# Kernel optimization log

Hardware: AMD Instinct MI355X
Metric: run time of the kernel (lower is better)

Reference implementation:

```python
import jax, jax.numpy as jnp
from jax import lax
import numpy as np

EPS = 1e-5

def _conv(x, w, b, s, p):
    # torch Conv2d: weight [O,I,kH,kW], NCHW
    y = lax.conv_general_dilated(x, w, (s, s), [(p, p), (p, p)],
                                 dimension_numbers=('NCHW', 'OIHW', 'NCHW'))
    return y + b[None, :, None, None]

def _convT(x, w, b, s, p):
    # torch ConvTranspose2d: weight [I,O,kH,kW]; equivalent to lhs-dilated conv
    wf = jnp.flip(w, (2, 3)).transpose(1, 0, 2, 3)  # -> [O,I,kH,kW]
    q = w.shape[2] - 1 - p
    y = lax.conv_general_dilated(x, wf, (1, 1), [(q, q), (q, q)],
                                 lhs_dilation=(s, s),
                                 dimension_numbers=('NCHW', 'OIHW', 'NCHW'))
    return y + b[None, :, None, None]

def _bn(x, g, b, m, v):
    # eval-mode BatchNorm2d with running stats
    s = g / jnp.sqrt(v + EPS)
    return x * s[None, :, None, None] + (b - m * s)[None, :, None, None]

def _forward(x, ew1, eb1, bn1g, bn1b, bn1m, bn1v, ew2, eb2, bn2g, bn2b, bn2m, bn2v,
             ew3, eb3, bn3g, bn3b, bn3m, bn3v, ew4, eb4, bn4g, bn4b, bn4m, bn4v,
             fc21w, fc21b, fc22w, fc22b, fc3w, fc3b,
             cw1, cb1, cbn1g, cbn1b, cbn1m, cbn1v, cw2, cb2, emb,
             dw1, db1, dbn1g, dbn1b, dbn1m, dbn1v, dw2, db2, dbn2g, dbn2b, dbn2m, dbn2v,
             dw3, db3, dbn3g, dbn3b, dbn3m, dbn3v, dw4, db4, dbn4g, dbn4b, dbn4m, dbn4v,
             ow, ob):
    relu = jax.nn.relu
    N = x.shape[0]
    # ---- encoder ----
    h = relu(_bn(_conv(x, ew1, eb1, 2, 1), bn1g, bn1b, bn1m, bn1v))   # [N,16,32,32]
    h = relu(_bn(_conv(h, ew2, eb2, 2, 1), bn2g, bn2b, bn2m, bn2v))   # [N,16,16,16]
    h = relu(_bn(_conv(h, ew3, eb3, 2, 1), bn3g, bn3b, bn3m, bn3v))   # [N,16,9,9]
    h = relu(_bn(_conv(h, ew4, eb4, 1, 0), bn4g, bn4b, bn4m, bn4v))   # [N,128,9,9]
    hl = h.reshape(N, -1)                                              # [N,10368]
    mu = hl @ fc21w + fc21b
    logvar = hl @ fc22w + fc22b
    z = mu  # eval-mode reparameterize returns mu
    # ---- vq_decode ----
    co = relu(z @ fc3w + fc3b)                                         # [N,10368]
    col = co.reshape(N, 128, 9, 9)
    ze = relu(_bn(_convT(col, cw1, cb1, 1, 0), cbn1g, cbn1b, cbn1m, cbn1v))
    z_e_x = _convT(ze, cw2, cb2, 1, 0)                                 # [N,32,9,9]
    zt = z_e_x.transpose(0, 2, 3, 1)                                   # [N,H,W,C]
    # ||z - e||^2 expanded (avoids [N,H,W,C,K] intermediate)
    d = ((zt * zt).sum(-1, keepdims=True)
         - 2.0 * jnp.einsum('nhwc,kc->nhwk', zt, emb)
         + (emb * emb).sum(-1))                                        # [N,H,W,K]
    latents = jnp.argmin(d, axis=-1)                                   # [N,H,W] int
    z_q = emb[latents]                                                 # [N,H,W,C]
    z_q_x = z_q.transpose(0, 3, 1, 2)                                  # [N,32,9,9]
    # ---- decoder ----
    g = relu(_bn(_convT(z_q_x, dw1, db1, 1, 0), dbn1g, dbn1b, dbn1m, dbn1v))  # [N,16,9,9]
    g = relu(_bn(_convT(g, dw2, db2, 2, 1), dbn2g, dbn2b, dbn2m, dbn2v))      # [N,16,18,18]
    g = relu(_bn(_convT(g, dw3, db3, 2, 1), dbn3g, dbn3b, dbn3m, dbn3v))      # [N,16,34,34]
    g = relu(_bn(_convT(g, dw4, db4, 2, 0), dbn4g, dbn4b, dbn4m, dbn4v))      # [N,16,68,68]
    x_tilde = _convT(g, ow, ob, 1, 0)                                         # [N,1,68,68]
    return (x_tilde, z, mu, logvar, z_e_x, z_q_x, latents)


def setup_inputs() -> dict:
    key = jax.random.key(0)
    ks = iter(jax.random.split(key, 64))
    def rn(shape, scale=0.05):
        return scale * jax.random.normal(next(ks), shape, jnp.float32)
    inp = {'x': jax.random.normal(next(ks), (512, 1, 64, 64), jnp.float32)}
    wspecs = {
        'ew1': (16, 1, 4, 4), 'eb1': (16,), 'ew2': (16, 16, 4, 4), 'eb2': (16,),
        'ew3': (16, 16, 2, 2), 'eb3': (16,), 'ew4': (128, 16, 1, 1), 'eb4': (128,),
        'fc21w': (10368, 64), 'fc21b': (64,), 'fc22w': (10368, 64), 'fc22b': (64,),
        'fc3w': (64, 10368), 'fc3b': (10368,),
        'cw1': (128, 32, 1, 1), 'cb1': (32,), 'cw2': (32, 32, 1, 1), 'cb2': (32,),
        'dw1': (32, 16, 1, 1), 'db1': (16,), 'dw2': (16, 16, 4, 4), 'db2': (16,),
        'dw3': (16, 16, 2, 2), 'db3': (16,), 'dw4': (16, 16, 2, 2), 'db4': (16,),
        'ow': (16, 1, 1, 1),
    }
    for n, s in wspecs.items():
        inp[n] = rn(s)
    inp['ob'] = jnp.full((1,), 0.5, jnp.float32)
    for ch, pre in [(16, 'bn1'), (16, 'bn2'), (16, 'bn3'), (128, 'bn4'), (32, 'cbn1'),
                    (16, 'dbn1'), (16, 'dbn2'), (16, 'dbn3'), (16, 'dbn4')]:
        inp[pre + 'g'] = jnp.ones((ch,), jnp.float32)
        inp[pre + 'b'] = jnp.zeros((ch,), jnp.float32)
        inp[pre + 'm'] = jnp.zeros((ch,), jnp.float32)
        inp[pre + 'v'] = jnp.ones((ch,), jnp.float32)
    inp['emb'] = rn((512, 32), 1.0 / 512)
    return inp


def reference(x, ew1, eb1, bn1g, bn1b, bn1m, bn1v, ew2, eb2, bn2g, bn2b, bn2m, bn2v,
              ew3, eb3, bn3g, bn3b, bn3m, bn3v, ew4, eb4, bn4g, bn4b, bn4m, bn4v,
              fc21w, fc21b, fc22w, fc22b, fc3w, fc3b,
              cw1, cb1, cbn1g, cbn1b, cbn1m, cbn1v, cw2, cb2, emb,
              dw1, db1, dbn1g, dbn1b, dbn1m, dbn1v, dw2, db2, dbn2g, dbn2b, dbn2m, dbn2v,
              dw3, db3, dbn3g, dbn3b, dbn3m, dbn3v, dw4, db4, dbn4g, dbn4b, dbn4m, dbn4v,
              ow, ob):
    return _forward(x, ew1, eb1, bn1g, bn1b, bn1m, bn1v, ew2, eb2, bn2g, bn2b, bn2m, bn2v,
                    ew3, eb3, bn3g, bn3b, bn3m, bn3v, ew4, eb4, bn4g, bn4b, bn4m, bn4v,
                    fc21w, fc21b, fc22w, fc22b, fc3w, fc3b,
                    cw1, cb1, cbn1g, cbn1b, cbn1m, cbn1v, cw2, cb2, emb,
                    dw1, db1, dbn1g, dbn1b, dbn1m, dbn1v, dw2, db2, dbn2g, dbn2b, dbn2m, dbn2v,
                    dw3, db3, dbn3g, dbn3b, dbn3m, dbn3v, dw4, db4, dbn4g, dbn4b, dbn4m, dbn4v,
                    ow, ob)
```

## Files before the change

kernel.cpp:

```cpp
#include <hip/hip_runtime.h>
#include <math.h>
#include <float.h>

#define BN_EPS 1e-5f

__device__ __forceinline__ float bn_apply(float y, float g, float b, float m, float v) {
  float s = g / sqrtf(v + BN_EPS);
  return y * s + (b - m * s);
}

__global__ void k_conv1(const float* __restrict__ x, const float* __restrict__ w,
                        const float* __restrict__ bias,
                        const float* __restrict__ g, const float* __restrict__ bb,
                        const float* __restrict__ bm, const float* __restrict__ bv,
                        float* __restrict__ out) {
  int t = blockIdx.x * 256 + threadIdx.x;
  int xo = t & 31, yo = (t >> 5) & 31, n = t >> 10;
  int iy0 = 2 * yo - 1, ix0 = 2 * xo - 1;
  const float* xb = x + n * 4096;
  float p[16];
#pragma unroll
  for (int ky = 0; ky < 4; ++ky)
#pragma unroll
    for (int kx = 0; kx < 4; ++kx) {
      int iy = iy0 + ky, ix = ix0 + kx;
      bool ok = (iy >= 0) & (iy < 64) & (ix >= 0) & (ix < 64);
      p[ky * 4 + kx] = ok ? xb[iy * 64 + ix] : 0.0f;
    }
  float* ob = out + n * 16384 + yo * 32 + xo;
#pragma unroll
  for (int o = 0; o < 16; ++o) {
    float acc = bias[o];
#pragma unroll
    for (int k = 0; k < 16; ++k) acc += p[k] * w[o * 16 + k];
    acc = bn_apply(acc, g[o], bb[o], bm[o], bv[o]);
    ob[o * 1024] = fmaxf(acc, 0.0f);
  }
}

__global__ void k_conv2(const float* __restrict__ A, const float* __restrict__ w,
                        const float* __restrict__ bias,
                        const float* __restrict__ g, const float* __restrict__ bb,
                        const float* __restrict__ bm, const float* __restrict__ bv,
                        float* __restrict__ out) {
  __shared__ float ws[4096];
  for (int i = threadIdx.x; i < 4096; i += 256) ws[i] = w[i];
  __syncthreads();
  int t = blockIdx.x * 256 + threadIdx.x;
  int x8 = t & 7, yo = (t >> 3) & 15, n = t >> 7;
  int iy0 = 2 * yo - 1;
  const float* Ab = A + n * 16384;
  float acc[2][16];
#pragma unroll
  for (int o = 0; o < 16; ++o) { float bvv = bias[o]; acc[0][o] = bvv; acc[1][o] = bvv; }
  for (int i = 0; i < 16; ++i) {
    float p[2][16];
#pragma unroll
    for (int px = 0; px < 2; ++px) {
      int ix0 = 2 * (x8 + px * 8) - 1;
#pragma unroll
      for (int ky = 0; ky < 4; ++ky)
#pragma unroll
        for (int kx = 0; kx < 4; ++kx) {
          int iy = iy0 + ky, ix = ix0 + kx;
          bool ok = (iy >= 0) & (iy < 32) & (ix >= 0) & (ix < 32);
          p[px][ky * 4 + kx] = ok ? Ab[i * 1024 + iy * 32 + ix] : 0.0f;
        }
    }
#pragma unroll
    for (int o = 0; o < 16; ++o) {
#pragma unroll
      for (int k = 0; k < 16; ++k) {
        float wv = ws[(o * 16 + i) * 16 + k];
        acc[0][o] += p[0][k] * wv;
        acc[1][o] += p[1][k] * wv;
      }
    }
  }
#pragma unroll
  for (int o = 0; o < 16; ++o) {
    float s = g[o] / sqrtf(bv[o] + BN_EPS);
    float sh = bb[o] - bm[o] * s;
    float* ob = out + (n * 16 + o) * 256 + yo * 16;
    ob[x8]     = fmaxf(acc[0][o] * s + sh, 0.0f);
    ob[x8 + 8] = fmaxf(acc[1][o] * s + sh, 0.0f);
  }
}

__global__ void __launch_bounds__(256) k_c34(const float* __restrict__ in,
    const float* __restrict__ w3, const float* __restrict__ b3,
    const float* __restrict__ g3, const float* __restrict__ bb3,
    const float* __restrict__ bm3, const float* __restrict__ bv3,
    const float* __restrict__ w4, const float* __restrict__ b4,
    const float* __restrict__ g4, const float* __restrict__ bb4,
    const float* __restrict__ bm4, const float* __restrict__ bv4,
    float* __restrict__ hl) {
  __shared__ float xin[4096];
  __shared__ float w3s[1024];
  __shared__ float c3s[16 * 81];
  __shared__ float k3a[16], k3b[16];
  __shared__ float k4a[128], k4b[128];
  int bx = blockIdx.x;
  int n = bx >> 1, half = bx & 1;
  int t = threadIdx.x;
  {
    const float4* iv = (const float4*)(in + n * 4096);
    float4* xv = (float4*)xin;
#pragma unroll
    for (int q = 0; q < 4; ++q) xv[t + 256 * q] = iv[t + 256 * q];
    for (int i = t; i < 1024; i += 256) w3s[i] = w3[i];
  }
  if (t < 16) {
    float s = g3[t] / sqrtf(bv3[t] + BN_EPS);
    k3a[t] = s;
    k3b[t] = b3[t] * s + (bb3[t] - bm3[t] * s);
  } else if (t >= 64 && t < 192) {
    int o = t - 64;
    float s = g4[o] / sqrtf(bv4[o] + BN_EPS);
    k4a[o] = s;
    k4b[o] = b4[o] * s + (bb4[o] - bm4[o] * s);
  }
  __syncthreads();
  for (int idx = t; idx < 1296; idx += 256) {
    int o = idx / 81, p = idx - o * 81;
    int yo = p / 9, xo = p - yo * 9;
    int iy0 = 2 * yo - 1, ix0 = 2 * xo - 1;
    bool ytop = iy0 >= 0, ybot = iy0 + 1 < 16;
    bool xlft = ix0 >= 0, xrgt = ix0 + 1 < 16;
    int iyt = ytop ? iy0 : 0, iyb = ybot ? iy0 + 1 : 15;
    int ixl = xlft ? ix0 : 0, ixr = xrgt ? ix0 + 1 : 15;
    float acc = 0.0f;
#pragma unroll
    for (int i = 0; i < 16; ++i) {
      const float* ch = xin + i * 256;
      float p0 = (ytop & xlft) ? ch[iyt * 16 + ixl] : 0.0f;
      float p1 = (ytop & xrgt) ? ch[iyt * 16 + ixr] : 0.0f;
      float p2 = (ybot & xlft) ? ch[iyb * 16 + ixl] : 0.0f;
      float p3 = (ybot & xrgt) ? ch[iyb * 16 + ixr] : 0.0f;
      float4 wv = *(const float4*)&w3s[(o * 16 + i) * 4];
      acc += p0 * wv.x + p1 * wv.y + p2 * wv.z + p3 * wv.w;
    }
    c3s[idx] = fmaxf(acc * k3a[o] + k3b[o], 0.0f);
  }
  __syncthreads();
  int lane = t & 63;
  int og = __builtin_amdgcn_readfirstlane(t >> 6);
  int o0 = half * 64 + og * 16;
  float* ob = hl + n * 10368;
#pragma unroll
  for (int pass = 0; pass < 2; ++pass) {
    int p = pass * 64 + lane;
    bool ok = p < 81; int pc = ok ? p : 80;
    float acc[16];
#pragma unroll
    for (int oo = 0; oo < 16; ++oo) acc[oo] = 0.0f;
#pragma unroll
    for (int i = 0; i < 16; ++i) {
      float v = c3s[i * 81 + pc];
#pragma unroll
      for (int oo = 0; oo < 16; ++oo)
        acc[oo] = fmaf(v, w4[(o0 + oo) * 16 + i], acc[oo]);
    }
    if (ok) {
#pragma unroll
      for (int oo = 0; oo < 16; ++oo) {
        int o = o0 + oo;
        ob[o * 81 + p] = fmaxf(acc[oo] * k4a[o] + k4b[o], 0.0f);
      }
    }
  }
}

__global__ void __launch_bounds__(256) k_gemm1(const float* __restrict__ hl,
                                               const float* __restrict__ w21,
                                               const float* __restrict__ w22,
                                               float* __restrict__ part) {
  __shared__ __align__(16) float hs[27 * 68];
  __shared__ __align__(16) float wsh[27 * 128];
  int kc = blockIdx.x, nt = blockIdx.y, t = threadIdx.x;
  int n0 = nt * 64, k0 = kc * 162;
  int jg = t & 31, ng = t >> 5;
  float acc[8][4];
#pragma unroll
  for (int i = 0; i < 8; ++i)
#pragma unroll
    for (int q = 0; q < 4; ++q) acc[i][q] = 0.0f;
  float ph[7], pw[14];
  {
    int ks = k0;
#pragma unroll
    for (int q = 0; q < 7; ++q) {
      int idx = t + q * 256;
      if (idx < 1728) { int nr = idx / 27, kk = idx - nr * 27;
        ph[q] = hl[(n0 + nr) * 10368 + ks + kk]; }
    }
#pragma unroll
    for (int q = 0; q < 14; ++q) {
      int idx = t + q * 256;
      if (idx < 3456) { int r = idx >> 7, c = idx & 127;
        pw[q] = (c < 64) ? w21[(ks + r) * 64 + c] : w22[(ks + r) * 64 + (c - 64)]; }
    }
  }
  for (int s = 0; s < 6; ++s) {
    __syncthreads();
#pragma unroll
    for (int q = 0; q < 7; ++q) {
      int idx = t + q * 256;
      if (idx < 1728) { int nr = idx / 27, kk = idx - nr * 27; hs[kk * 68 + nr] = ph[q]; }
    }
#pragma unroll
    for (int q = 0; q < 14; ++q) {
      int idx = t + q * 256;
      if (idx < 3456) wsh[idx] = pw[q];
    }
    __syncthreads();
    if (s < 5) {
      int ks = k0 + (s + 1) * 27;
#pragma unroll
      for (int q = 0; q < 7; ++q) {
        int idx = t + q * 256;
        if (idx < 1728) { int nr = idx / 27, kk = idx - nr * 27;
          ph[q] = hl[(n0 + nr) * 10368 + ks + kk]; }
      }
#pragma unroll
      for (int q = 0; q < 14; ++q) {
        int idx = t + q * 256;
        if (idx < 3456) { int r = idx >> 7, c = idx & 127;
          pw[q] = (c < 64) ? w21[(ks + r) * 64 + c] : w22[(ks + r) * 64 + (c - 64)]; }
      }
    }
#pragma unroll 9
    for (int kk = 0; kk < 27; ++kk) {
      float4 h0 = *(const float4*)&hs[kk * 68 + ng * 8];
      float4 h1 = *(const float4*)&hs[kk * 68 + ng * 8 + 4];
      float4 wv = *(const float4*)&wsh[kk * 128 + jg * 4];
      float hv[8] = {h0.x, h0.y, h0.z, h0.w, h1.x, h1.y, h1.z, h1.w};
#pragma unroll
      for (int i = 0; i < 8; ++i) {
        acc[i][0] = fmaf(hv[i], wv.x, acc[i][0]);
        acc[i][1] = fmaf(hv[i], wv.y, acc[i][1]);
        acc[i][2] = fmaf(hv[i], wv.z, acc[i][2]);
        acc[i][3] = fmaf(hv[i], wv.w, acc[i][3]);
      }
    }
  }
#pragma unroll
  for (int i = 0; i < 8; ++i) {
    int n = n0 + ng * 8 + i;
    *(float4*)&part[(size_t)(kc * 512 + n) * 128 + jg * 4] =
        make_float4(acc[i][0], acc[i][1], acc[i][2], acc[i][3]);
  }
}

__global__ void k_fc_red(const float* __restrict__ part, const float* __restrict__ b21,
                         const float* __restrict__ b22, float* __restrict__ z,
                         float* __restrict__ mu, float* __restrict__ lv) {
  int t = blockIdx.x * 256 + threadIdx.x;
  int j = t & 127, n = t >> 7;
  float s = 0.0f;
  for (int kc = 0; kc < 64; ++kc) s += part[(size_t)(kc * 512 + n) * 128 + j];
  if (j < 64) { float r = s + b21[j]; z[n * 64 + j] = r; mu[n * 64 + j] = r; }
  else        { lv[n * 64 + (j - 64)] = s + b22[j - 64]; }
}

__global__ void k_fc3(const float* __restrict__ z, const float* __restrict__ w,
                      const float* __restrict__ b, float* __restrict__ E) {
  int m = blockIdx.x * 128 + threadIdx.x;
  int n0 = blockIdx.y * 32;
  float acc[32];
#pragma unroll
  for (int nn = 0; nn < 32; ++nn) acc[nn] = 0.0f;
  for (int j = 0; j < 64; ++j) {
    float wv = w[j * 10368 + m];
    const float* zb = z + n0 * 64 + j;
#pragma unroll
    for (int nn = 0; nn < 32; ++nn) acc[nn] += zb[nn * 64] * wv;
  }
  float bvv = b[m];
  float* Eb = E + n0 * 10368 + m;
#pragma unroll
  for (int nn = 0; nn < 32; ++nn) Eb[nn * 10368] = fmaxf(acc[nn] + bvv, 0.0f);
}

__global__ void __launch_bounds__(256) k_cw(const float* __restrict__ E,
                     const float* __restrict__ w1, const float* __restrict__ b1,
                     const float* __restrict__ g, const float* __restrict__ bb,
                     const float* __restrict__ bm, const float* __restrict__ bv,
                     const float* __restrict__ w2, const float* __restrict__ b2,
                     float* __restrict__ zex, float* __restrict__ zt) {
  __shared__ float ze_s[2592];
  int n = blockIdx.x, t = threadIdx.x;
  int lane = t & 63;
  int o0 = __builtin_amdgcn_readfirstlane(t >> 6) * 8;
  const float* co = E + n * 10368;
#pragma unroll
  for (int pass = 0; pass < 2; ++pass) {
    int p = pass * 64 + lane;
    bool ok = p < 81; int pc = ok ? p : 80;
    float acc[8];
#pragma unroll
    for (int oo = 0; oo < 8; ++oo) acc[oo] = b1[o0 + oo];
    for (int i = 0; i < 128; ++i) {
      float v = co[i * 81 + pc];
#pragma unroll
      for (int oo = 0; oo < 8; ++oo)
        acc[oo] = fmaf(v, w1[i * 32 + o0 + oo], acc[oo]);
    }
#pragma unroll
    for (int oo = 0; oo < 8; ++oo) {
      int o = o0 + oo;
      float r = bn_apply(acc[oo], g[o], bb[o], bm[o], bv[o]);
      if (ok) ze_s[o * 81 + p] = fmaxf(r, 0.0f);
    }
  }
  __syncthreads();
  float* zb = zex + n * 2592;
  float* ztb = zt + n * 81 * 32;
#pragma unroll
  for (int pass = 0; pass < 2; ++pass) {
    int p = pass * 64 + lane;
    bool ok = p < 81; int pc = ok ? p : 80;
    float acc[8];
#pragma unroll
    for (int oo = 0; oo < 8; ++oo) acc[oo] = b2[o0 + oo];
    for (int j = 0; j < 32; ++j) {
      float v = ze_s[j * 81 + pc];
#pragma unroll
      for (int oo = 0; oo < 8; ++oo)
        acc[oo] = fmaf(v, w2[j * 32 + o0 + oo], acc[oo]);
    }
    if (ok) {
#pragma unroll
      for (int oo = 0; oo < 8; ++oo) {
        zb[(o0 + oo) * 81 + p] = acc[oo];
        ztb[p * 32 + o0 + oo] = acc[oo];
      }
    }
  }
}

__global__ void k_ee(const float* __restrict__ emb, float* __restrict__ ee) {
  int k = blockIdx.x * 256 + threadIdx.x;
  if (k < 512) {
    const float4* e = (const float4*)(emb + k * 32);
    float s = 0.0f;
#pragma unroll
    for (int q = 0; q < 8; ++q) {
      float4 v = e[q];
      s += v.x * v.x + v.y * v.y + v.z * v.z + v.w * v.w;
    }
    ee[k] = s;
  }
}

__global__ void __launch_bounds__(256) k_vq2(const float* __restrict__ zt,
                                             const float* __restrict__ emb,
                                             const float* __restrict__ ee,
                                             float* __restrict__ lat_out,
                                             float* __restrict__ zqx) {
  __shared__ float bd_s[4][64];
  __shared__ int   bi_s[4][64];
  __shared__ int   bif[64];
  int t = threadIdx.x;
  int lane = t & 63, sub = t >> 6;
  int sub_u = __builtin_amdgcn_readfirstlane(sub);
  int pix = blockIdx.x * 64 + lane;
  float z[32];
  {
    const float4* zr = (const float4*)(zt + (size_t)pix * 32);
#pragma unroll
    for (int q = 0; q < 8; ++q) {
      float4 v = zr[q];
      z[q * 4] = v.x; z[q * 4 + 1] = v.y; z[q * 4 + 2] = v.z; z[q * 4 + 3] = v.w;
    }
  }
  const float* ebase = emb + sub_u * 128 * 32;
  const float* eeb   = ee + sub_u * 128;
  int kbase = sub_u * 128;
  float best = FLT_MAX;
  int bi = kbase;
  for (int kk = 0; kk < 128; kk += 2) {
    const float* e0 = ebase + kk * 32;
    const float* e1 = e0 + 32;
    float d0a = 0.f, d0b = 0.f, d1a = 0.f, d1b = 0.f;
#pragma unroll
    for (int c = 0; c < 32; c += 2) {
      d0a = fmaf(z[c], e0[c], d0a);
      d0b = fmaf(z[c + 1], e0[c + 1], d0b);
      d1a = fmaf(z[c], e1[c], d1a);
      d1b = fmaf(z[c + 1], e1[c + 1], d1b);
    }
    float d0 = fmaf(-2.0f, d0a + d0b, eeb[kk]);
    float d1 = fmaf(-2.0f, d1a + d1b, eeb[kk + 1]);
    if (d0 < best) { best = d0; bi = kbase + kk; }
    if (d1 < best) { best = d1; bi = kbase + kk + 1; }
  }
  bd_s[sub][lane] = best;
  bi_s[sub][lane] = bi;
  __syncthreads();
  if (t < 64) {
    float bd = bd_s[0][t]; int b = bi_s[0][t];
#pragma unroll
    for (int q = 1; q < 4; ++q)
      if (bd_s[q][t] < bd) { bd = bd_s[q][t]; b = bi_s[q][t]; }
    lat_out[blockIdx.x * 64 + t] = (float)b;
    bif[t] = b;
  }
  __syncthreads();
  int pix0 = blockIdx.x * 64;
  for (int idx = t; idx < 2048; idx += 256) {
    int c = idx >> 6, pl = idx & 63;
    int pg = pix0 + pl;
    int n = pg / 81, p = pg - n * 81;
    zqx[n * 2592 + c * 81 + p] = emb[bif[pl] * 32 + c];
  }
}

__global__ void k_dw1(const float* __restrict__ in, const float* __restrict__ w,
                      const float* __restrict__ bias,
                      const float* __restrict__ g, const float* __restrict__ bb,
                      const float* __restrict__ bm, const float* __restrict__ bv,
                      float* __restrict__ out) {
  __shared__ float ws[512];
  for (int i = threadIdx.x; i < 512; i += 256) ws[i] = w[i];
  __syncthreads();
  int t = blockIdx.x * 256 + threadIdx.x;
  int p = t % 81; int o = (t / 81) & 15; int n = t / 1296;
  const float* ib = in + n * 2592 + p;
  float acc = bias[o];
#pragma unroll
  for (int i = 0; i < 32; ++i) acc += ib[i * 81] * ws[i * 16 + o];
  float r = bn_apply(acc, g[o], bb[o], bm[o], bv[o]);
  out[t] = fmaxf(r, 0.0f);
}

__global__ void __launch_bounds__(256) k_dw2(const float* __restrict__ in,
                      const float* __restrict__ w, const float* __restrict__ bias,
                      const float* __restrict__ g, const float* __restrict__ bb,
                      const float* __restrict__ bm, const float* __restrict__ bv,
                      float* __restrict__ out) {
  int t = threadIdx.x;
  int lane = t & 63;
  int og = __builtin_amdgcn_readfirstlane(t >> 6);
  int idx = blockIdx.x * 64 + lane;
  int n = idx / 81, blk = idx - n * 81;
  int iy = blk / 9, ix = blk - iy * 9;
  const float* ib = in + n * 1296;
  int r0 = iy - 1, r2 = iy + 1, c0 = ix - 1, c2 = ix + 1;
  bool r0ok = r0 >= 0, r2ok = r2 < 9, c0ok = c0 >= 0, c2ok = c2 < 9;
  int r0c = r0ok ? r0 : 0, r2c = r2ok ? r2 : 8;
  int c0c = c0ok ? c0 : 0, c2c = c2ok ? c2 : 8;
  float acc[4][2][2];
#pragma unroll
  for (int oo = 0; oo < 4; ++oo)
#pragma unroll
    for (int dy = 0; dy < 2; ++dy)
#pragma unroll
      for (int dx = 0; dx < 2; ++dx) acc[oo][dy][dx] = 0.0f;
  for (int i = 0; i < 16; ++i) {
    const float* ch = ib + i * 81;
    float v[3][3];
    v[1][1] = ch[iy * 9 + ix];
    v[1][0] = c0ok ? ch[iy * 9 + c0c] : 0.0f;
    v[1][2] = c2ok ? ch[iy * 9 + c2c] : 0.0f;
    v[0][1] = r0ok ? ch[r0c * 9 + ix] : 0.0f;
    v[0][0] = (r0ok & c0ok) ? ch[r0c * 9 + c0c] : 0.0f;
    v[0][2] = (r0ok & c2ok) ? ch[r0c * 9 + c2c] : 0.0f;
    v[2][1] = r2ok ? ch[r2c * 9 + ix] : 0.0f;
    v[2][0] = (r2ok & c0ok) ? ch[r2c * 9 + c0c] : 0.0f;
    v[2][2] = (r2ok & c2ok) ? ch[r2c * 9 + c2c] : 0.0f;
    const float* wb = w + (i * 16 + og * 4) * 16;
#pragma unroll
    for (int oo = 0; oo < 4; ++oo) {
      const float* wo = wb + oo * 16;
      acc[oo][0][0] = fmaf(v[1][1], wo[1 * 4 + 1], acc[oo][0][0]);
      acc[oo][0][0] = fmaf(v[1][0], wo[1 * 4 + 3], acc[oo][0][0]);
      acc[oo][0][0] = fmaf(v[0][1], wo[3 * 4 + 1], acc[oo][0][0]);
      acc[oo][0][0] = fmaf(v[0][0], wo[3 * 4 + 3], acc[oo][0][0]);
      acc[oo][0][1] = fmaf(v[1][1], wo[1 * 4 + 2], acc[oo][0][1]);
      acc[oo][0][1] = fmaf(v[1][2], wo[1 * 4 + 0], acc[oo][0][1]);
      acc[oo][0][1] = fmaf(v[0][1], wo[3 * 4 + 2], acc[oo][0][1]);
      acc[oo][0][1] = fmaf(v[0][2], wo[3 * 4 + 0], acc[oo][0][1]);
      acc[oo][1][0] = fmaf(v[1][1], wo[2 * 4 + 1], acc[oo][1][0]);
      acc[oo][1][0] = fmaf(v[1][0], wo[2 * 4 + 3], acc[oo][1][0]);
      acc[oo][1][0] = fmaf(v[2][1], wo[0 * 4 + 1], acc[oo][1][0]);
      acc[oo][1][0] = fmaf(v[2][0], wo[0 * 4 + 3], acc[oo][1][0]);
      acc[oo][1][1] = fmaf(v[1][1], wo[2 * 4 + 2], acc[oo][1][1]);
      acc[oo][1][1] = fmaf(v[1][2], wo[2 * 4 + 0], acc[oo][1][1]);
      acc[oo][1][1] = fmaf(v[2][1], wo[0 * 4 + 2], acc[oo][1][1]);
      acc[oo][1][1] = fmaf(v[2][2], wo[0 * 4 + 0], acc[oo][1][1]);
    }
  }
  float* ob = out + n * 5184 + (2 * iy) * 18 + 2 * ix;
#pragma unroll
  for (int oo = 0; oo < 4; ++oo) {
    int o = og * 4 + oo;
    float s = g[o] / sqrtf(bv[o] + BN_EPS);
    float sh = bb[o] - bm[o] * s;
    float bo = bias[o];
    float r00 = fmaxf((acc[oo][0][0] + bo) * s + sh, 0.0f);
    float r01 = fmaxf((acc[oo][0][1] + bo) * s + sh, 0.0f);
    float r10 = fmaxf((acc[oo][1][0] + bo) * s + sh, 0.0f);
    float r11 = fmaxf((acc[oo][1][1] + bo) * s + sh, 0.0f);
    float* op = ob + o * 324;
    *(float2*)&op[0]  = make_float2(r00, r01);
    *(float2*)&op[18] = make_float2(r10, r11);
  }
}

__global__ void k_dw3(const float* __restrict__ in, const float* __restrict__ w,
                      const float* __restrict__ bias,
                      const float* __restrict__ g, const float* __restrict__ bb,
                      const float* __restrict__ bm, const float* __restrict__ bv,
                      float* __restrict__ out) {
  int t = blockIdx.x * 256 + threadIdx.x;
  int ii = t % 324; int n = t / 324;
  int iy = ii / 18, ix = ii % 18;
  const float* ib = in + n * 5184 + iy * 18 + ix;
  float acc[4][16];
#pragma unroll
  for (int a = 0; a < 4; ++a)
#pragma unroll
    for (int o = 0; o < 16; ++o) acc[a][o] = 0.0f;
  for (int i = 0; i < 16; ++i) {
    float v = ib[i * 324];
    const float4* wr = (const float4*)(w + i * 64);
#pragma unroll
    for (int o = 0; o < 16; ++o) {
      float4 wt = wr[o];
      acc[0][o] = fmaf(v, wt.x, acc[0][o]);
      acc[1][o] = fmaf(v, wt.y, acc[1][o]);
      acc[2][o] = fmaf(v, wt.z, acc[2][o]);
      acc[3][o] = fmaf(v, wt.w, acc[3][o]);
    }
  }
  int yo0 = 2 * iy - 1, xo0 = 2 * ix - 1;
  float* ob = out + n * 18496;
#pragma unroll
  for (int o = 0; o < 16; ++o) {
    float s = g[o] / sqrtf(bv[o] + BN_EPS);
    float sh = bb[o] - bm[o] * s;
    float bo = bias[o];
#pragma unroll
    for (int a = 0; a < 2; ++a)
#pragma unroll
      for (int b = 0; b < 2; ++b) {
        int yo = yo0 + a, xo = xo0 + b;
        if (yo >= 0 && yo < 34 && xo >= 0 && xo < 34)
          ob[o * 1156 + yo * 34 + xo] = fmaxf((acc[a * 2 + b][o] + bo) * s + sh, 0.0f);
      }
  }
}

__global__ void k_dw4ow(const float* __restrict__ in, const float* __restrict__ w,
                        const float* __restrict__ bias,
                        const float* __restrict__ g, const float* __restrict__ bb,
                        const float* __restrict__ bm, const float* __restrict__ bv,
                        const float* __restrict__ oww, const float* __restrict__ obb,
                        float* __restrict__ out) {
  int t = blockIdx.x * 256 + threadIdx.x;
  int ii = t % 1156; int n = t / 1156;
  int iy = ii / 34, ix = ii % 34;
  const float* ib = in + n * 18496 + iy * 34 + ix;
  float acc[4][16];
#pragma unroll
  for (int a = 0; a < 4; ++a)
#pragma unroll
    for (int o = 0; o < 16; ++o) acc[a][o] = 0.0f;
  for (int i = 0; i < 16; ++i) {
    float v = ib[i * 1156];
    const float4* wr = (const float4*)(w + i * 64);
#pragma unroll
    for (int o = 0; o < 16; ++o) {
      float4 wt = wr[o];
      acc[0][o] = fmaf(v, wt.x, acc[0][o]);
      acc[1][o] = fmaf(v, wt.y, acc[1][o]);
      acc[2][o] = fmaf(v, wt.z, acc[2][o]);
      acc[3][o] = fmaf(v, wt.w, acc[3][o]);
    }
  }
  float r[4];
#pragma unroll
  for (int a = 0; a < 4; ++a) r[a] = obb[0];
#pragma unroll
  for (int o = 0; o < 16; ++o) {
    float s = g[o] / sqrtf(bv[o] + BN_EPS);
    float sh = bb[o] - bm[o] * s;
    float bo = bias[o];
    float wo = oww[o];
#pragma unroll
    for (int a = 0; a < 4; ++a)
      r[a] += fmaxf((acc[a][o] + bo) * s + sh, 0.0f) * wo;
  }
  float* ob = out + n * 4624 + 2 * ix;
  *(float2*)&ob[(2 * iy) * 68]     = make_float2(r[0], r[1]);
  *(float2*)&ob[(2 * iy + 1) * 68] = make_float2(r[2], r[3]);
}

extern "C" void kernel_launch(void* const* d_in, const int* in_sizes, int n_in,
                              void* d_out, int out_size, void* d_ws, size_t ws_size,
                              hipStream_t stream) {
  const float* x     = (const float*)d_in[0];
  const float* ew1   = (const float*)d_in[1];
  const float* eb1   = (const float*)d_in[2];
  const float* ew2   = (const float*)d_in[3];
  const float* eb2   = (const float*)d_in[4];
  const float* ew3   = (const float*)d_in[5];
  const float* eb3   = (const float*)d_in[6];
  const float* ew4   = (const float*)d_in[7];
  const float* eb4   = (const float*)d_in[8];
  const float* fc21w = (const float*)d_in[9];
  const float* fc21b = (const float*)d_in[10];
  const float* fc22w = (const float*)d_in[11];
  const float* fc22b = (const float*)d_in[12];
  const float* fc3w  = (const float*)d_in[13];
  const float* fc3b  = (const float*)d_in[14];
  const float* cw1   = (const float*)d_in[15];
  const float* cb1   = (const float*)d_in[16];
  const float* cw2   = (const float*)d_in[17];
  const float* cb2   = (const float*)d_in[18];
  const float* dw1   = (const float*)d_in[19];
  const float* db1   = (const float*)d_in[20];
  const float* dw2   = (const float*)d_in[21];
  const float* db2   = (const float*)d_in[22];
  const float* dw3   = (const float*)d_in[23];
  const float* db3   = (const float*)d_in[24];
  const float* dw4   = (const float*)d_in[25];
  const float* db4   = (const float*)d_in[26];
  const float* oww   = (const float*)d_in[27];
  const float* obb   = (const float*)d_in[28];
  const float* bn1g  = (const float*)d_in[29];
  const float* bn1b  = (const float*)d_in[30];
  const float* bn1m  = (const float*)d_in[31];
  const float* bn1v  = (const float*)d_in[32];
  const float* bn2g  = (const float*)d_in[33];
  const float* bn2b  = (const float*)d_in[34];
  const float* bn2m  = (const float*)d_in[35];
  const float* bn2v  = (const float*)d_in[36];
  const float* bn3g  = (const float*)d_in[37];
  const float* bn3b  = (const float*)d_in[38];
  const float* bn3m  = (const float*)d_in[39];
  const float* bn3v  = (const float*)d_in[40];
  const float* bn4g  = (const float*)d_in[41];
  const float* bn4b  = (const float*)d_in[42];
  const float* bn4m  = (const float*)d_in[43];
  const float* bn4v  = (const float*)d_in[44];
  const float* cbn1g = (const float*)d_in[45];
  const float* cbn1b = (const float*)d_in[46];
  const float* cbn1m = (const float*)d_in[47];
  const float* cbn1v = (const float*)d_in[48];
  const float* dbn1g = (const float*)d_in[49];
  const float* dbn1b = (const float*)d_in[50];
  const float* dbn1m = (const float*)d_in[51];
  const float* dbn1v = (const float*)d_in[52];
  const float* dbn2g = (const float*)d_in[53];
  const float* dbn2b = (const float*)d_in[54];
  const float* dbn2m = (const float*)d_in[55];
  const float* dbn2v = (const float*)d_in[56];
  const float* dbn3g = (const float*)d_in[57];
  const float* dbn3b = (const float*)d_in[58];
  const float* dbn3m = (const float*)d_in[59];
  const float* dbn3v = (const float*)d_in[60];
  const float* dbn4g = (const float*)d_in[61];
  const float* dbn4b = (const float*)d_in[62];
  const float* dbn4m = (const float*)d_in[63];
  const float* dbn4v = (const float*)d_in[64];
  const float* emb   = (const float*)d_in[65];

  float* out = (float*)d_out;
  float* xt_o  = out;
  float* z_o   = out + 2367488;
  float* mu_o  = out + 2400256;
  float* lv_o  = out + 2433024;
  float* zex_o = out + 2465792;
  float* zqx_o = out + 3792896;
  float* lat_o = out + 5120000;

  float* ws = (float*)d_ws;
  float* A    = ws;
  float* Bt   = ws + 8388608;
  float* Dhl  = ws + 663552;
  float* part = ws + 5971968;
  float* Eco  = ws;
  float* zt   = ws + 10166272;
  float* eev  = ws + 11493376;
  float* G    = ws + 5308416;
  float* H    = ws + 5971968;
  float* I    = ws + 8626176;

  k_conv1<<<2048, 256, 0, stream>>>(x, ew1, eb1, bn1g, bn1b, bn1m, bn1v, A);
  k_conv2<<<256, 256, 0, stream>>>(A, ew2, eb2, bn2g, bn2b, bn2m, bn2v, Bt);
  k_c34<<<1024, 256, 0, stream>>>(Bt, ew3, eb3, bn3g, bn3b, bn3m, bn3v,
                                  ew4, eb4, bn4g, bn4b, bn4m, bn4v, Dhl);
  k_gemm1<<<dim3(64, 8), 256, 0, stream>>>(Dhl, fc21w, fc22w, part);
  k_fc_red<<<256, 256, 0, stream>>>(part, fc21b, fc22b, z_o, mu_o, lv_o);
  k_ee<<<2, 256, 0, stream>>>(emb, eev);
  k_fc3<<<dim3(81, 16), 128, 0, stream>>>(z_o, fc3w, fc3b, Eco);
  k_cw<<<512, 256, 0, stream>>>(Eco, cw1, cb1, cbn1g, cbn1b, cbn1m, cbn1v, cw2, cb2, zex_o, zt);
  k_vq2<<<648, 256, 0, stream>>>(zt, emb, eev, lat_o, zqx_o);
  k_dw1<<<2592, 256, 0, stream>>>(zqx_o, dw1, db1, dbn1g, dbn1b, dbn1m, dbn1v, G);
  k_dw2<<<648, 256, 0, stream>>>(G, dw2, db2, dbn2g, dbn2b, dbn2m, dbn2v, H);
  k_dw3<<<648, 256, 0, stream>>>(H, dw3, db3, dbn3g, dbn3b, dbn3m, dbn3v, I);
  k_dw4ow<<<2312, 256, 0, stream>>>(I, dw4, db4, dbn4g, dbn4b, dbn4m, dbn4v, oww, obb, xt_o);
}
```

Before: 486.9 us.

## Stage padded conv2 input tiles in shared memory and split work across more blocks

```diff
diff --git a/kernel.cpp b/kernel.cpp
--- a/kernel.cpp
+++ b/kernel.cpp
@@ -38,52 +38,51 @@
   }
 }
 
-__global__ void k_conv2(const float* __restrict__ A, const float* __restrict__ w,
-                        const float* __restrict__ bias,
+__global__ void __launch_bounds__(128) k_conv2(const float* __restrict__ A,
+                        const float* __restrict__ w, const float* __restrict__ bias,
                         const float* __restrict__ g, const float* __restrict__ bb,
                         const float* __restrict__ bm, const float* __restrict__ bv,
                         float* __restrict__ out) {
-  __shared__ float ws[4096];
-  for (int i = threadIdx.x; i < 4096; i += 256) ws[i] = w[i];
+  __shared__ float xin[16 * 612];
+  int bx = blockIdx.x;
+  int n = bx >> 1, h = bx & 1;
+  int t = threadIdx.x;
+  const float* Ab = A + n * 16384;
+  for (int idx = t; idx < 9792; idx += 128) {
+    int i = idx / 612, rem = idx - i * 612;
+    int r = rem / 34, c = rem - r * 34;
+    int gr = 16 * h - 1 + r, gc = c - 1;
+    bool ok = (gr >= 0) & (gr < 32) & (gc >= 0) & (gc < 32);
+    xin[idx] = ok ? Ab[i * 1024 + gr * 32 + gc] : 0.0f;
+  }
   __syncthreads();
-  int t = blockIdx.x * 256 + threadIdx.x;
-  int x8 = t & 7, yo = (t >> 3) & 15, n = t >> 7;
-  int iy0 = 2 * yo - 1;
-  const float* Ab = A + n * 16384;
-  float acc[2][16];
-#pragma unroll
-  for (int o = 0; o < 16; ++o) { float bvv = bias[o]; acc[0][o] = bvv; acc[1][o] = bvv; }
+  int yl = t >> 4, xo = t & 15;
+  float acc[16];
+#pragma unroll
+  for (int o = 0; o < 16; ++o) acc[o] = bias[o];
   for (int i = 0; i < 16; ++i) {
-    float p[2][16];
-#pragma unroll
-    for (int px = 0; px < 2; ++px) {
-      int ix0 = 2 * (x8 + px * 8) - 1;
-#pragma unroll
-      for (int ky = 0; ky < 4; ++ky)
-#pragma unroll
-        for (int kx = 0; kx < 4; ++kx) {
-          int iy = iy0 + ky, ix = ix0 + kx;
-          bool ok = (iy >= 0) & (iy < 32) & (ix >= 0) & (ix < 32);
-          p[px][ky * 4 + kx] = ok ? Ab[i * 1024 + iy * 32 + ix] : 0.0f;
-        }
-    }
+    const float* ch = xin + i * 612 + yl * 68 + 2 * xo;
+    float p[16];
+#pragma unroll
+    for (int ky = 0; ky < 4; ++ky)
+#pragma unroll
+      for (int kx = 0; kx < 4; ++kx)
+        p[ky * 4 + kx] = ch[ky * 34 + kx];
+    const float* wi = w + i * 16;
 #pragma unroll
     for (int o = 0; o < 16; ++o) {
-#pragma unroll
-      for (int k = 0; k < 16; ++k) {
-        float wv = ws[(o * 16 + i) * 16 + k];
-        acc[0][o] += p[0][k] * wv;
-        acc[1][o] += p[1][k] * wv;
-      }
-    }
-  }
+      const float* wo = wi + o * 256;
+#pragma unroll
+      for (int k = 0; k < 16; ++k) acc[o] = fmaf(p[k], wo[k], acc[o]);
+    }
+  }
+  int yo = 8 * h + yl;
+  float* ob = out + n * 4096 + yo * 16 + xo;
 #pragma unroll
   for (int o = 0; o < 16; ++o) {
     float s = g[o] / sqrtf(bv[o] + BN_EPS);
     float sh = bb[o] - bm[o] * s;
-    float* ob = out + (n * 16 + o) * 256 + yo * 16;
-    ob[x8]     = fmaxf(acc[0][o] * s + sh, 0.0f);
-    ob[x8 + 8] = fmaxf(acc[1][o] * s + sh, 0.0f);
+    ob[o * 256] = fmaxf(acc[o] * s + sh, 0.0f);
   }
 }
 
@@ -689,7 +688,7 @@
   float* I    = ws + 8626176;
 
   k_conv1<<<2048, 256, 0, stream>>>(x, ew1, eb1, bn1g, bn1b, bn1m, bn1v, A);
-  k_conv2<<<256, 256, 0, stream>>>(A, ew2, eb2, bn2g, bn2b, bn2m, bn2v, Bt);
+  k_conv2<<<1024, 128, 0, stream>>>(A, ew2, eb2, bn2g, bn2b, bn2m, bn2v, Bt);
   k_c34<<<1024, 256, 0, stream>>>(Bt, ew3, eb3, bn3g, bn3b, bn3m, bn3v,
                                   ew4, eb4, bn4g, bn4b, bn4m, bn4v, Dhl);
   k_gemm1<<<dim3(64, 8), 256, 0, stream>>>(Dhl, fc21w, fc22w, part);
```

Result: slower. 526.4 us (+8.1%).

## Repartition conv2 across output-channel groups per wave for higher occupancy

Applied to the files above, without the earlier changes.

```diff
diff --git a/kernel.cpp b/kernel.cpp
--- a/kernel.cpp
+++ b/kernel.cpp
@@ -38,52 +38,48 @@
   }
 }
 
-__global__ void k_conv2(const float* __restrict__ A, const float* __restrict__ w,
-                        const float* __restrict__ bias,
+__global__ void __launch_bounds__(256) k_conv2(const float* __restrict__ A,
+                        const float* __restrict__ w, const float* __restrict__ bias,
                         const float* __restrict__ g, const float* __restrict__ bb,
                         const float* __restrict__ bm, const float* __restrict__ bv,
                         float* __restrict__ out) {
-  __shared__ float ws[4096];
-  for (int i = threadIdx.x; i < 4096; i += 256) ws[i] = w[i];
-  __syncthreads();
-  int t = blockIdx.x * 256 + threadIdx.x;
-  int x8 = t & 7, yo = (t >> 3) & 15, n = t >> 7;
-  int iy0 = 2 * yo - 1;
+  int t = threadIdx.x;
+  int lane = t & 63;
+  int og = __builtin_amdgcn_readfirstlane(t >> 6);
+  int idx = blockIdx.x * 64 + lane;
+  int n = idx >> 8, p = idx & 255;
+  int yo = p >> 4, xo = p & 15;
+  int iy0 = 2 * yo - 1, ix0 = 2 * xo - 1;
   const float* Ab = A + n * 16384;
-  float acc[2][16];
-#pragma unroll
-  for (int o = 0; o < 16; ++o) { float bvv = bias[o]; acc[0][o] = bvv; acc[1][o] = bvv; }
+  float acc[4];
+#pragma unroll
+  for (int oo = 0; oo < 4; ++oo) acc[oo] = bias[og * 4 + oo];
   for (int i = 0; i < 16; ++i) {
-    float p[2][16];
-#pragma unroll
-    for (int px = 0; px < 2; ++px) {
-      int ix0 = 2 * (x8 + px * 8) - 1;
-#pragma unroll
-      for (int ky = 0; ky < 4; ++ky)
-#pragma unroll
-        for (int kx = 0; kx < 4; ++kx) {
-          int iy = iy0 + ky, ix = ix0 + kx;
-          bool ok = (iy >= 0) & (iy < 32) & (ix >= 0) & (ix < 32);
-          p[px][ky * 4 + kx] = ok ? Ab[i * 1024 + iy * 32 + ix] : 0.0f;
-        }
-    }
-#pragma unroll
-    for (int o = 0; o < 16; ++o) {
-#pragma unroll
-      for (int k = 0; k < 16; ++k) {
-        float wv = ws[(o * 16 + i) * 16 + k];
-        acc[0][o] += p[0][k] * wv;
-        acc[1][o] += p[1][k] * wv;
+    const float* ch = Ab + i * 1024;
+    float pv[16];
+#pragma unroll
+    for (int ky = 0; ky < 4; ++ky)
+#pragma unroll
+      for (int kx = 0; kx < 4; ++kx) {
+        int iy = iy0 + ky, ix = ix0 + kx;
+        bool ok = (iy >= 0) & (iy < 32) & (ix >= 0) & (ix < 32);
+        pv[ky * 4 + kx] = ok ? ch[iy * 32 + ix] : 0.0f;
       }
-    }
-  }
-#pragma unroll
-  for (int o = 0; o < 16; ++o) {
+    const float* wb = w + ((og * 4) * 16 + i) * 16;
+#pragma unroll
+    for (int oo = 0; oo < 4; ++oo) {
+      const float* wo = wb + oo * 256;
+#pragma unroll
+      for (int k = 0; k < 16; ++k) acc[oo] = fmaf(pv[k], wo[k], acc[oo]);
+    }
+  }
+  float* ob = out + n * 4096 + p;
+#pragma unroll
+  for (int oo = 0; oo < 4; ++oo) {
+    int o = og * 4 + oo;
     float s = g[o] / sqrtf(bv[o] + BN_EPS);
     float sh = bb[o] - bm[o] * s;
-    float* ob = out + (n * 16 + o) * 256 + yo * 16;
-    ob[x8]     = fmaxf(acc[0][o] * s + sh, 0.0f);
-    ob[x8 + 8] = fmaxf(acc[1][o] * s + sh, 0.0f);
+    ob[o * 256] = fmaxf(acc[oo] * s + sh, 0.0f);
   }
 }
 
@@ -689,7 +685,7 @@
   float* I    = ws + 8626176;
 
   k_conv1<<<2048, 256, 0, stream>>>(x, ew1, eb1, bn1g, bn1b, bn1m, bn1v, A);
-  k_conv2<<<256, 256, 0, stream>>>(A, ew2, eb2, bn2g, bn2b, bn2m, bn2v, Bt);
+  k_conv2<<<2048, 256, 0, stream>>>(A, ew2, eb2, bn2g, bn2b, bn2m, bn2v, Bt);
   k_c34<<<1024, 256, 0, stream>>>(Bt, ew3, eb3, bn3g, bn3b, bn3m, bn3v,
                                   ew4, eb4, bn4g, bn4b, bn4m, bn4v, Dhl);
   k_gemm1<<<dim3(64, 8), 256, 0, stream>>>(Dhl, fc21w, fc22w, part);
```

Result: no change. 488.4 us (+0.3%).
